# Performance work log

Hardware: AMD Instinct MI355X
Metric: run time of the kernel (lower is better)

The kernel has to match this reference:

```python
import jax, jax.numpy as jnp
import numpy as np

B, S, H, NS, HEADS, L = 16, 1024, 1024, 32, 16, 5
DH = H // HEADS
LN_EPS = 1e-7


def setup_inputs() -> dict:
    key = jax.random.key(0)
    ks = jax.random.split(key, 12)
    std = 0.02
    inp = {
        "encoder_layer": jax.random.normal(ks[0], (B, S, H), jnp.float32),
        "lstm_W_ih": jax.random.normal(ks[1], (4 * H, H), jnp.float32) * std,
        "lstm_W_hh": jax.random.normal(ks[2], (4 * H, H), jnp.float32) * std,
        "lstm_b_ih": jnp.zeros((4 * H,), jnp.float32),
        "lstm_b_hh": jnp.zeros((4 * H,), jnp.float32),
        "ln_gamma": jnp.ones((H,), jnp.float32),
        "ln_beta": jnp.zeros((H,), jnp.float32),
        "Wq": jax.random.normal(ks[3], (H, H), jnp.float32) * std,
        "bq": jnp.zeros((H,), jnp.float32),
        "Wk": jax.random.normal(ks[4], (H, H), jnp.float32) * std,
        "bk": jnp.zeros((H,), jnp.float32),
        "Wv": jax.random.normal(ks[5], (H, H), jnp.float32) * std,
        "bv": jnp.zeros((H,), jnp.float32),
        "Wo": jax.random.normal(ks[6], (H, H), jnp.float32) * std,
        "bo": jnp.zeros((H,), jnp.float32),
        "attn_ln_gamma": jnp.ones((H,), jnp.float32),
        "attn_ln_beta": jnp.zeros((H,), jnp.float32),
        "clf_W": jax.random.normal(ks[7], (L, H), jnp.float32) * std,
        "clf_b": jnp.zeros((L,), jnp.float32),
    }
    # contiguous ragged spans: head_j = 32*j, tail_j = 32*(j+1); slice is head+1:tail
    seg = S // NS
    heads = jnp.tile(jnp.arange(NS, dtype=jnp.int32)[None, :] * seg, (B, 1))
    inp["span_head_idxs"] = heads
    inp["span_tail_idxs"] = heads + seg
    inp["span_attention_mask"] = jnp.ones((B, NS), jnp.int32)
    return inp


def _layer_norm(x, gamma, beta):
    mu = jnp.mean(x, axis=-1, keepdims=True)
    var = jnp.mean(jnp.square(x - mu), axis=-1, keepdims=True)
    return (x - mu) * jax.lax.rsqrt(var + LN_EPS) * gamma + beta


def reference(encoder_layer, lstm_W_ih, lstm_W_hh, lstm_b_ih, lstm_b_hh,
              ln_gamma, ln_beta, Wq, bq, Wk, bk, Wv, bv, Wo, bo,
              attn_ln_gamma, attn_ln_beta, clf_W, clf_b,
              span_head_idxs, span_tail_idxs, span_attention_mask):
    # --- unidirectional LSTM over the sequence (torch gate order i,f,g,o) ---
    x_tbh = jnp.swapaxes(encoder_layer, 0, 1)  # [S,B,H]
    h0 = jnp.zeros((B, H), encoder_layer.dtype)
    c0 = jnp.zeros((B, H), encoder_layer.dtype)

    def step(carry, xt):
        h, c = carry
        gates = xt @ lstm_W_ih.T + lstm_b_ih + h @ lstm_W_hh.T + lstm_b_hh
        i, f, g, o = jnp.split(gates, 4, axis=-1)
        i, f, o = jax.nn.sigmoid(i), jax.nn.sigmoid(f), jax.nn.sigmoid(o)
        c = f * c + i * jnp.tanh(g)
        h = o * jnp.tanh(c)
        return (h, c), h

    _, hs = jax.lax.scan(step, (h0, c0), x_tbh)
    enc = jnp.swapaxes(hs, 0, 1)  # [B,S,H]

    # --- ragged span mean pooling (tokens head+1 .. tail-1) via masked matmul ---
    t = jnp.arange(S, dtype=jnp.int32)  # [S]
    span_mask = ((t[None, None, :] >= span_head_idxs[:, :, None] + 1)
                 & (t[None, None, :] < span_tail_idxs[:, :, None]))  # [B,NS,S]
    mf = span_mask.astype(enc.dtype)
    sums = jnp.einsum('bns,bsh->bnh', mf, enc)
    counts = jnp.sum(mf, axis=-1, keepdims=True)
    mean_vec = sums / counts  # [B,NS,H]

    mean_vec = _layer_norm(mean_vec, ln_gamma, ln_beta)

    # --- DeBERTa-style self-attention (relative_attention=False) over spans ---
    m2d = (span_attention_mask[:, None, None, :]
           * span_attention_mask[:, None, :, None])  # [B,1,NS,NS]
    mbool = m2d.astype(bool)

    def split_heads(y):
        return jnp.swapaxes(y.reshape(B, NS, HEADS, DH), 1, 2)  # [B,h,NS,dh]

    q = split_heads(mean_vec @ Wq.T + bq)
    k = split_heads(mean_vec @ Wk.T + bk)
    v = split_heads(mean_vec @ Wv.T + bv)
    scale = jnp.sqrt(jnp.asarray(DH, mean_vec.dtype))
    scores = jnp.einsum('bhqd,bhkd->bhqk', q, k) / scale
    scores = jnp.where(mbool, scores, jnp.finfo(scores.dtype).min)
    probs = jax.nn.softmax(scores, axis=-1)
    probs = jnp.where(mbool, probs, 0.0)  # XSoftmax zeroes masked positions
    ctx = jnp.einsum('bhqk,bhkd->bhqd', probs, v)
    ctx = jnp.swapaxes(ctx, 1, 2).reshape(B, NS, H)
    attn_out = _layer_norm(ctx @ Wo.T + bo + mean_vec, attn_ln_gamma, attn_ln_beta)

    # dropout is identity in eval mode
    logits = attn_out @ clf_W.T + clf_b  # [B,NS,L]
    return logits
```

## Files before the change

### kernel.cpp

```cpp
#include <hip/hip_runtime.h>
#include <hip/hip_bf16.h>

#define DEV __device__ __forceinline__

typedef __attribute__((ext_vector_type(8))) short short8;
typedef __attribute__((ext_vector_type(4))) float f32x4;
typedef __attribute__((ext_vector_type(4))) unsigned int u32x4;

static constexpr int B_ = 16, S_ = 1024, H_ = 1024, NS_ = 32, HEADS_ = 16, L_ = 5;
static constexpr int G4H = 4096;
static constexpr int LSTM_GRID = 64;

DEV unsigned short f2bf(float f){
  union { float f; unsigned int i; } u; u.f = f;
  unsigned int r = (u.i + 0x7fffu + ((u.i >> 16) & 1u)) >> 16;
  return (unsigned short)r;
}
DEV float bf2f(unsigned short h){
  union { unsigned int i; float f; } u; u.i = ((unsigned int)h) << 16;
  return u.f;
}
DEV float sigm(float x){ return 1.f / (1.f + __expf(-x)); }
DEV float tanh_(float x){
  x = fminf(30.f, fmaxf(-30.f, x));
  float e = __expf(-2.f * x);
  return (1.f - e) / (1.f + e);
}

DEV u32x4 load_coh16(const void* p){
  u32x4 r;
  asm volatile("global_load_dwordx4 %0, %1, off sc0 sc1" : "=v"(r) : "v"(p));
  return r;
}
DEV void store_coh16(void* p, u32x4 v){
  asm volatile("global_store_dwordx4 %0, %1, off sc0 sc1" :: "v"(p), "v"(v) : "memory");
}

__global__ void k_spanof(const int* __restrict__ head, const int* __restrict__ tail,
                         int* __restrict__ spanof){
  const int b = blockIdx.x;
  for (int t = threadIdx.x; t < S_; t += blockDim.x) spanof[b * S_ + t] = -1;
  __syncthreads();
  if (threadIdx.x < NS_){
    const int n = threadIdx.x;
    const int h = head[b * NS_ + n], tl = tail[b * NS_ + n];
    for (int t = h + 1; t < tl; ++t) spanof[b * S_ + t] = n;
  }
}

__global__ __launch_bounds__(256) void k_gates(const float* __restrict__ enc,
    const float* __restrict__ Wih, const float* __restrict__ bih,
    const float* __restrict__ bhh, unsigned short* __restrict__ gx){
  const int nb = blockIdx.x;
  const int mb = blockIdx.y;
  __shared__ __align__(16) unsigned short As[128 * 40];
  __shared__ __align__(16) unsigned short Bs[128 * 40];
  const int tid = threadIdx.x, w = tid >> 6, l = tid & 63;
  const int wm = (w >> 1) * 64, wn = (w & 1) * 64;
  const int cl = l & 15, bg = l >> 4;
  f32x4 acc[4][4] = {};
  const int t0 = mb * 8, n0 = nb * 128;
  const int srow = tid >> 1, skq = (tid & 1) * 16;
  const int sb = srow & 15, stt = t0 + (srow >> 4);
  const float* Asrc = enc + ((size_t)sb * S_ + stt) * H_ + skq;
  const float* Bsrc = Wih + (size_t)(n0 + srow) * H_ + skq;
  for (int k0 = 0; k0 < H_; k0 += 32){
    #pragma unroll
    for (int q = 0; q < 4; ++q){
      float4 a = *(const float4*)(Asrc + k0 + q * 4);
      float4 b = *(const float4*)(Bsrc + k0 + q * 4);
      ushort4 ua; ua.x = f2bf(a.x); ua.y = f2bf(a.y); ua.z = f2bf(a.z); ua.w = f2bf(a.w);
      ushort4 ub; ub.x = f2bf(b.x); ub.y = f2bf(b.y); ub.z = f2bf(b.z); ub.w = f2bf(b.w);
      *(ushort4*)(As + srow * 40 + skq + q * 4) = ua;
      *(ushort4*)(Bs + srow * 40 + skq + q * 4) = ub;
    }
    __syncthreads();
    short8 af[4], bf[4];
    const int kq = bg * 8;
    #pragma unroll
    for (int i = 0; i < 4; ++i) af[i] = *(const short8*)(As + (wm + i * 16 + cl) * 40 + kq);
    #pragma unroll
    for (int i = 0; i < 4; ++i) bf[i] = *(const short8*)(Bs + (wn + i * 16 + cl) * 40 + kq);
    #pragma unroll
    for (int mi = 0; mi < 4; ++mi)
      #pragma unroll
      for (int ni = 0; ni < 4; ++ni)
        acc[mi][ni] = __builtin_amdgcn_mfma_f32_16x16x32_bf16(af[mi], bf[ni], acc[mi][ni], 0, 0, 0);
    __syncthreads();
  }
  #pragma unroll
  for (int ni = 0; ni < 4; ++ni){
    const int c = n0 + wn + ni * 16 + cl;
    const float bias = bih[c] + bhh[c];
    const int g = c >> 10, j = c & 1023;
    const int cuq = j >> 4, wq = (j >> 2) & 3, jjq = j & 3;
    const int nq = jjq * 4 + g;
    #pragma unroll
    for (int mi = 0; mi < 4; ++mi){
      const int tg = t0 + ((wm + mi * 16) >> 4);
      ushort4 o;
      o.x = f2bf(acc[mi][ni].x + bias);
      o.y = f2bf(acc[mi][ni].y + bias);
      o.z = f2bf(acc[mi][ni].z + bias);
      o.w = f2bf(acc[mi][ni].w + bias);
      const size_t u4i = (((size_t)tg * 64 + cuq) * 64 + (wq * 16 + nq)) * 4 + bg;
      *((ushort4*)gx + u4i) = o;
    }
  }
}

__global__ __launch_bounds__(256, 1) void k_lstm(const float* __restrict__ Whh,
    const unsigned short* __restrict__ gx, const int* __restrict__ spanof,
    unsigned short* __restrict__ hbuf, unsigned int* __restrict__ tags,
    float* __restrict__ sums){
  __shared__ __align__(16) unsigned char Himg[32768];
  __shared__ __align__(16) unsigned short Hs[256];
  const int cu = blockIdx.x, tid = threadIdx.x;
  const int w = tid >> 6, l = tid & 63;
  const int n = l & 15, bg = l >> 4;
  const int g = n & 3, jj = n >> 2;
  const int j = cu * 16 + w * 4 + jj;
  const int bstar = bg * 4 + g;
  const int jl = w * 4 + jj;

  short8 wr[32];
  {
    const float* wsrc = Whh + (size_t)(g * H_ + j) * H_ + bg * 8;
    #pragma unroll
    for (int kk = 0; kk < 32; ++kk){
      float4 x = *(const float4*)(wsrc + kk * 32);
      float4 y = *(const float4*)(wsrc + kk * 32 + 4);
      short8 v;
      v[0] = (short)f2bf(x.x); v[1] = (short)f2bf(x.y);
      v[2] = (short)f2bf(x.z); v[3] = (short)f2bf(x.w);
      v[4] = (short)f2bf(y.x); v[5] = (short)f2bf(y.y);
      v[6] = (short)f2bf(y.z); v[7] = (short)f2bf(y.w);
      wr[kk] = v;
    }
  }

  const unsigned int abase = (unsigned)(n * 2048 + bg * 16);
  const unsigned int aswz  = (unsigned)((n & 7) << 4);

  const ushort4* gxp = (const ushort4*)gx + ((size_t)cu * 64 + w * 16 + n) * 4 + bg;
  const int* sp = spanof + (size_t)bstar * S_;

  float cstate = 0.f, pool = 0.f;
  int curspan = -1;

  for (int t = 0; t < S_; ++t){
    const int p = t & 1;
    const ushort4 gxv = gxp[(size_t)t * 16384];
    const int s = sp[t];
    {
      const unsigned int* tp = tags + (size_t)p * 1024 + (size_t)l * 16;
      unsigned int v = __hip_atomic_load(tp, __ATOMIC_RELAXED, __HIP_MEMORY_SCOPE_AGENT);
      int guard = 0;
      while (!__all(v == (unsigned int)t)){
        __builtin_amdgcn_s_sleep(1);
        v = __hip_atomic_load(tp, __ATOMIC_RELAXED, __HIP_MEMORY_SCOPE_AGENT);
        if (++guard > 2000000) break;
      }
    }
    {
      const unsigned char* hsrc = (const unsigned char*)hbuf + p * 32768 + w * 8192 + l * 16;
      u32x4 v0 = load_coh16(hsrc + 0 * 1024);
      u32x4 v1 = load_coh16(hsrc + 1 * 1024);
      u32x4 v2 = load_coh16(hsrc + 2 * 1024);
      u32x4 v3 = load_coh16(hsrc + 3 * 1024);
      u32x4 v4 = load_coh16(hsrc + 4 * 1024);
      u32x4 v5 = load_coh16(hsrc + 5 * 1024);
      u32x4 v6 = load_coh16(hsrc + 6 * 1024);
      u32x4 v7 = load_coh16(hsrc + 7 * 1024);
      asm volatile("s_waitcnt vmcnt(0)" ::: "memory");
      __builtin_amdgcn_sched_barrier(0);
      unsigned char* hdst = Himg + w * 8192 + l * 16;
      *(u32x4*)(hdst + 0 * 1024) = v0;
      *(u32x4*)(hdst + 1 * 1024) = v1;
      *(u32x4*)(hdst + 2 * 1024) = v2;
      *(u32x4*)(hdst + 3 * 1024) = v3;
      *(u32x4*)(hdst + 4 * 1024) = v4;
      *(u32x4*)(hdst + 5 * 1024) = v5;
      *(u32x4*)(hdst + 6 * 1024) = v6;
      *(u32x4*)(hdst + 7 * 1024) = v7;
    }
    __syncthreads();
    f32x4 a0 = {0,0,0,0}, a1 = {0,0,0,0}, a2 = {0,0,0,0}, a3 = {0,0,0,0};
    #pragma unroll
    for (int kk = 0; kk < 32; kk += 4){
      short8 h0 = *(const short8*)(Himg + ((abase + (kk + 0) * 64) ^ aswz));
      a0 = __builtin_amdgcn_mfma_f32_16x16x32_bf16(h0, wr[kk + 0], a0, 0, 0, 0);
      short8 h1 = *(const short8*)(Himg + ((abase + (kk + 1) * 64) ^ aswz));
      a1 = __builtin_amdgcn_mfma_f32_16x16x32_bf16(h1, wr[kk + 1], a1, 0, 0, 0);
      short8 h2 = *(const short8*)(Himg + ((abase + (kk + 2) * 64) ^ aswz));
      a2 = __builtin_amdgcn_mfma_f32_16x16x32_bf16(h2, wr[kk + 2], a2, 0, 0, 0);
      short8 h3 = *(const short8*)(Himg + ((abase + (kk + 3) * 64) ^ aswz));
      a3 = __builtin_amdgcn_mfma_f32_16x16x32_bf16(h3, wr[kk + 3], a3, 0, 0, 0);
    }
    f32x4 acc = (a0 + a1) + (a2 + a3);
    const float x0 = acc.x + bf2f(gxv.x);
    const float x1 = acc.y + bf2f(gxv.y);
    const float x2 = acc.z + bf2f(gxv.z);
    const float x3 = acc.w + bf2f(gxv.w);
    const float s1 = (g==0)?x1:(g==1)?x0:(g==2)?x3:x2;
    const float s2 = (g==0)?x2:(g==1)?x3:(g==2)?x0:x1;
    const float s3 = (g==0)?x3:(g==1)?x2:(g==2)?x1:x0;
    const float r1 = __shfl_xor(s1, 1, 64);
    const float r2 = __shfl_xor(s2, 2, 64);
    const float r3 = __shfl_xor(s3, 3, 64);
    const float own = (g==0)?x0:(g==1)?x1:(g==2)?x2:x3;
    const float vi = (g==0)?own:(g==1)?r1:(g==2)?r2:r3;
    const float vf = (g==1)?own:(g==0)?r1:(g==3)?r2:r3;
    const float vg = (g==2)?own:(g==3)?r1:(g==0)?r2:r3;
    const float vo = (g==3)?own:(g==2)?r1:(g==1)?r2:r3;
    const float ig = sigm(vi), fg = sigm(vf), gt = tanh_(vg), og = sigm(vo);
    cstate = fg * cstate + ig * gt;
    const float hval = og * tanh_(cstate);
    Hs[bstar * 16 + jl] = f2bf(hval);
    __syncthreads();
    if (tid < 32){
      const int sb = tid >> 1, half = tid & 1;
      const unsigned key = (unsigned)((sb & 7) << 4);
      const unsigned off = (unsigned)(sb * 2048)
          + ((unsigned)(cu * 32) ^ (key & 0x60))
          + ((unsigned)(half * 16) ^ (key & 0x10));
      u32x4 v = *(const u32x4*)((const unsigned char*)Hs + tid * 16);
      store_coh16((unsigned char*)hbuf + (p ^ 1) * 32768 + off, v);
    }
    if (tid == 0){
      asm volatile("s_waitcnt vmcnt(0)" ::: "memory");
      __hip_atomic_store(tags + (size_t)((t + 1) & 1) * 1024 + (size_t)cu * 16,
                         (unsigned int)(t + 1), __ATOMIC_RELAXED, __HIP_MEMORY_SCOPE_AGENT);
    }
    if (s != curspan){
      if (curspan >= 0) sums[((size_t)bstar * NS_ + curspan) * H_ + j] = pool;
      pool = 0.f; curspan = s;
    }
    if (s >= 0) pool += hval;
  }
  if (curspan >= 0) sums[((size_t)bstar * NS_ + curspan) * H_ + j] = pool;
}

DEV float block_sum(float v, float* red, int tid){
  #pragma unroll
  for (int d = 1; d < 64; d <<= 1) v += __shfl_xor(v, d, 64);
  if ((tid & 63) == 0) red[tid >> 6] = v;
  __syncthreads();
  const float r = red[0] + red[1] + red[2] + red[3];
  __syncthreads();
  return r;
}

__global__ __launch_bounds__(256) void k_poolln(const float* __restrict__ sums,
    const int* __restrict__ head, const int* __restrict__ tail,
    const float* __restrict__ gamma, const float* __restrict__ beta,
    unsigned short* __restrict__ mvb, float* __restrict__ mvf){
  __shared__ float red[4];
  const int m = blockIdx.x, tid = threadIdx.x;
  const float inv = 1.f / (float)(tail[m] - head[m] - 1);
  float4 x = *(const float4*)(sums + (size_t)m * H_ + tid * 4);
  x.x *= inv; x.y *= inv; x.z *= inv; x.w *= inv;
  const float mu = block_sum(x.x + x.y + x.z + x.w, red, tid) * (1.f / (float)H_);
  const float d0 = x.x - mu, d1 = x.y - mu, d2 = x.z - mu, d3 = x.w - mu;
  const float var = block_sum(d0*d0 + d1*d1 + d2*d2 + d3*d3, red, tid) * (1.f / (float)H_);
  const float rs = rsqrtf(var + 1e-7f);
  float4 gm = *(const float4*)(gamma + tid * 4);
  float4 bt = *(const float4*)(beta + tid * 4);
  float4 o; o.x = d0*rs*gm.x + bt.x; o.y = d1*rs*gm.y + bt.y;
  o.z = d2*rs*gm.z + bt.z; o.w = d3*rs*gm.w + bt.w;
  *(float4*)(mvf + (size_t)m * H_ + tid * 4) = o;
  ushort4 u; u.x = f2bf(o.x); u.y = f2bf(o.y); u.z = f2bf(o.z); u.w = f2bf(o.w);
  *(ushort4*)(mvb + (size_t)m * H_ + tid * 4) = u;
}

template<int OUT_BF16>
__global__ __launch_bounds__(256) void k_gemm2(const unsigned short* __restrict__ A,
    const float* __restrict__ Bw, const float* __restrict__ bias,
    float* __restrict__ Cf, unsigned short* __restrict__ Cb, int Nn){
  const int nb = blockIdx.x, mb = blockIdx.y;
  __shared__ __align__(16) unsigned short As[128 * 40];
  __shared__ __align__(16) unsigned short Bs[128 * 40];
  const int tid = threadIdx.x, w = tid >> 6, l = tid & 63;
  const int wm = (w >> 1) * 64, wn = (w & 1) * 64;
  const int cl = l & 15, bg = l >> 4;
  f32x4 acc[4][4] = {};
  const int m0 = mb * 128, n0 = nb * 128;
  const int srow = tid >> 1, skq = (tid & 1) * 16;
  const unsigned short* Asrc = A + (size_t)(m0 + srow) * 1024 + skq;
  const float* Bsrc = Bw + (size_t)(n0 + srow) * 1024 + skq;
  for (int k0 = 0; k0 < 1024; k0 += 32){
    uint4 av0 = *(const uint4*)(Asrc + k0);
    uint4 av1 = *(const uint4*)(Asrc + k0 + 8);
    *(uint4*)(As + srow * 40 + skq) = av0;
    *(uint4*)(As + srow * 40 + skq + 8) = av1;
    #pragma unroll
    for (int q = 0; q < 4; ++q){
      float4 b = *(const float4*)(Bsrc + k0 + q * 4);
      ushort4 ub; ub.x = f2bf(b.x); ub.y = f2bf(b.y); ub.z = f2bf(b.z); ub.w = f2bf(b.w);
      *(ushort4*)(Bs + srow * 40 + skq + q * 4) = ub;
    }
    __syncthreads();
    short8 af[4], bf[4];
    const int kq = bg * 8;
    #pragma unroll
    for (int i = 0; i < 4; ++i) af[i] = *(const short8*)(As + (wm + i * 16 + cl) * 40 + kq);
    #pragma unroll
    for (int i = 0; i < 4; ++i) bf[i] = *(const short8*)(Bs + (wn + i * 16 + cl) * 40 + kq);
    #pragma unroll
    for (int mi = 0; mi < 4; ++mi)
      #pragma unroll
      for (int ni = 0; ni < 4; ++ni)
        acc[mi][ni] = __builtin_amdgcn_mfma_f32_16x16x32_bf16(af[mi], bf[ni], acc[mi][ni], 0, 0, 0);
    __syncthreads();
  }
  #pragma unroll
  for (int ni = 0; ni < 4; ++ni){
    const int c = n0 + wn + ni * 16 + cl;
    const float bsv = bias ? bias[c] : 0.f;
    #pragma unroll
    for (int mi = 0; mi < 4; ++mi){
      const int m = m0 + wm + mi * 16 + bg * 4;
      const float v0 = acc[mi][ni].x + bsv, v1 = acc[mi][ni].y + bsv;
      const float v2 = acc[mi][ni].z + bsv, v3 = acc[mi][ni].w + bsv;
      if (OUT_BF16){
        Cb[(size_t)(m + 0) * Nn + c] = f2bf(v0);
        Cb[(size_t)(m + 1) * Nn + c] = f2bf(v1);
        Cb[(size_t)(m + 2) * Nn + c] = f2bf(v2);
        Cb[(size_t)(m + 3) * Nn + c] = f2bf(v3);
      } else {
        Cf[(size_t)(m + 0) * Nn + c] = v0;
        Cf[(size_t)(m + 1) * Nn + c] = v1;
        Cf[(size_t)(m + 2) * Nn + c] = v2;
        Cf[(size_t)(m + 3) * Nn + c] = v3;
      }
    }
  }
}

__global__ __launch_bounds__(256) void k_attn(const unsigned short* __restrict__ qb,
    const unsigned short* __restrict__ kb, const unsigned short* __restrict__ vb,
    const int* __restrict__ mask, unsigned short* __restrict__ ctx){
  const int bh = blockIdx.x, b = bh >> 4, hd = bh & 15;
  __shared__ float Q[32][64], K[32][64], V[32][64], Sc[32][33];
  __shared__ int msk[32];
  const int tid = threadIdx.x;
  const int row = tid >> 3, d0 = (tid & 7) * 8;
  {
    const size_t base = (size_t)(b * NS_ + row) * H_ + hd * 64 + d0;
    uint4 vq = *(const uint4*)(qb + base);
    uint4 vk = *(const uint4*)(kb + base);
    uint4 vv = *(const uint4*)(vb + base);
    const unsigned int wq[4] = {vq.x, vq.y, vq.z, vq.w};
    const unsigned int wk[4] = {vk.x, vk.y, vk.z, vk.w};
    const unsigned int wv[4] = {vv.x, vv.y, vv.z, vv.w};
    #pragma unroll
    for (int i = 0; i < 4; ++i){
      Q[row][d0 + 2*i]     = bf2f((unsigned short)(wq[i] & 0xffff));
      Q[row][d0 + 2*i + 1] = bf2f((unsigned short)(wq[i] >> 16));
      K[row][d0 + 2*i]     = bf2f((unsigned short)(wk[i] & 0xffff));
      K[row][d0 + 2*i + 1] = bf2f((unsigned short)(wk[i] >> 16));
      V[row][d0 + 2*i]     = bf2f((unsigned short)(wv[i] & 0xffff));
      V[row][d0 + 2*i + 1] = bf2f((unsigned short)(wv[i] >> 16));
    }
  }
  if (tid < 32) msk[tid] = mask[b * NS_ + tid];
  __syncthreads();
  {
    const int qi = tid >> 3, kb0 = (tid & 7) * 4;
    for (int kk = kb0; kk < kb0 + 4; ++kk){
      float s = 0.f;
      #pragma unroll
      for (int d = 0; d < 64; ++d) s += Q[qi][d] * K[kk][d];
      s *= 0.125f;
      if (!msk[qi] || !msk[kk]) s = -3.402823466e38f;
      Sc[qi][kk] = s;
    }
  }
  __syncthreads();
  if (tid < 32){
    float mx = -3.402823466e38f;
    for (int kk = 0; kk < 32; ++kk) mx = fmaxf(mx, Sc[tid][kk]);
    float sum = 0.f;
    for (int kk = 0; kk < 32; ++kk){
      const float e = __expf(Sc[tid][kk] - mx);
      Sc[tid][kk] = e; sum += e;
    }
    const float isum = 1.f / sum;
    for (int kk = 0; kk < 32; ++kk){
      float pv = Sc[tid][kk] * isum;
      if (!msk[tid] || !msk[kk]) pv = 0.f;
      Sc[tid][kk] = pv;
    }
  }
  __syncthreads();
  float o[8] = {0,0,0,0,0,0,0,0};
  for (int kk = 0; kk < 32; ++kk){
    const float p = Sc[row][kk];
    #pragma unroll
    for (int i = 0; i < 8; ++i) o[i] += p * V[kk][d0 + i];
  }
  ushort4 oA, oB;
  oA.x = f2bf(o[0]); oA.y = f2bf(o[1]); oA.z = f2bf(o[2]); oA.w = f2bf(o[3]);
  oB.x = f2bf(o[4]); oB.y = f2bf(o[5]); oB.z = f2bf(o[6]); oB.w = f2bf(o[7]);
  unsigned short* cp = ctx + (size_t)(b * NS_ + row) * H_ + hd * 64 + d0;
  *(ushort4*)(cp) = oA;
  *(ushort4*)(cp + 4) = oB;
}

__global__ __launch_bounds__(256) void k_residln(const float* __restrict__ wo,
    const float* __restrict__ mvf, const float* __restrict__ gamma,
    const float* __restrict__ beta, float* __restrict__ aof){
  __shared__ float red[4];
  const int m = blockIdx.x, tid = threadIdx.x;
  float4 a = *(const float4*)(wo + (size_t)m * H_ + tid * 4);
  float4 r = *(const float4*)(mvf + (size_t)m * H_ + tid * 4);
  float4 x; x.x = a.x + r.x; x.y = a.y + r.y; x.z = a.z + r.z; x.w = a.w + r.w;
  const float mu = block_sum(x.x + x.y + x.z + x.w, red, tid) * (1.f / (float)H_);
  const float d0 = x.x - mu, d1 = x.y - mu, d2 = x.z - mu, d3 = x.w - mu;
  const float var = block_sum(d0*d0 + d1*d1 + d2*d2 + d3*d3, red, tid) * (1.f / (float)H_);
  const float rs = rsqrtf(var + 1e-7f);
  float4 gm = *(const float4*)(gamma + tid * 4);
  float4 bt = *(const float4*)(beta + tid * 4);
  float4 o; o.x = d0*rs*gm.x + bt.x; o.y = d1*rs*gm.y + bt.y;
  o.z = d2*rs*gm.z + bt.z; o.w = d3*rs*gm.w + bt.w;
  *(float4*)(aof + (size_t)m * H_ + tid * 4) = o;
}

__global__ __launch_bounds__(64) void k_clf(const float* __restrict__ ao,
    const float* __restrict__ Wc, const float* __restrict__ bc, float* __restrict__ out){
  const int m = blockIdx.x, l = threadIdx.x;
  const float* a = ao + (size_t)m * H_ + l * 16;
  float av[16];
  #pragma unroll
  for (int i = 0; i < 4; ++i){
    float4 v = *(const float4*)(a + i * 4);
    av[i*4+0] = v.x; av[i*4+1] = v.y; av[i*4+2] = v.z; av[i*4+3] = v.w;
  }
  float p[5];
  #pragma unroll
  for (int c = 0; c < 5; ++c){
    const float* wr = Wc + (size_t)c * H_ + l * 16;
    float s = 0.f;
    #pragma unroll
    for (int i = 0; i < 4; ++i){
      float4 v = *(const float4*)(wr + i * 4);
      s += av[i*4+0]*v.x + av[i*4+1]*v.y + av[i*4+2]*v.z + av[i*4+3]*v.w;
    }
    p[c] = s;
  }
  #pragma unroll
  for (int d = 1; d < 64; d <<= 1){
    #pragma unroll
    for (int c = 0; c < 5; ++c) p[c] += __shfl_xor(p[c], d, 64);
  }
  if (l == 0){
    #pragma unroll
    for (int c = 0; c < 5; ++c) out[m * L_ + c] = p[c] + bc[c];
  }
}

extern "C" void kernel_launch(void* const* d_in, const int* in_sizes, int n_in,
                              void* d_out, int out_size, void* d_ws, size_t ws_size,
                              hipStream_t stream){
  (void)in_sizes; (void)n_in; (void)out_size; (void)ws_size;
  const float* enc  = (const float*)d_in[0];
  const float* Wih  = (const float*)d_in[1];
  const float* Whh  = (const float*)d_in[2];
  const float* bih  = (const float*)d_in[3];
  const float* bhh  = (const float*)d_in[4];
  const float* lng  = (const float*)d_in[5];
  const float* lnb  = (const float*)d_in[6];
  const float* Wq   = (const float*)d_in[7];
  const float* bq   = (const float*)d_in[8];
  const float* Wk   = (const float*)d_in[9];
  const float* bk   = (const float*)d_in[10];
  const float* Wv   = (const float*)d_in[11];
  const float* bv   = (const float*)d_in[12];
  const float* Wo   = (const float*)d_in[13];
  const float* bo   = (const float*)d_in[14];
  const float* alng = (const float*)d_in[15];
  const float* alnb = (const float*)d_in[16];
  const float* clfW = (const float*)d_in[17];
  const float* clfb = (const float*)d_in[18];
  const int* shead  = (const int*)d_in[19];
  const int* stail  = (const int*)d_in[20];
  const int* smask  = (const int*)d_in[21];
  float* out = (float*)d_out;
  unsigned char* ws = (unsigned char*)d_ws;

  size_t cur = 0;
  auto alloc = [&](size_t sz){ size_t r = cur; cur = (cur + sz + 255) & ~(size_t)255; return r; };
  const size_t off_gx   = alloc((size_t)S_ * G4H * B_ * 2);
  const size_t off_hbuf = alloc(2 * (size_t)B_ * H_ * 2);
  const size_t off_tags = alloc(2 * 1024 * 4);
  const size_t off_span = alloc((size_t)B_ * S_ * 4);
  const size_t off_sums = alloc((size_t)B_ * NS_ * H_ * 4);
  const size_t off_mvb  = alloc((size_t)B_ * NS_ * H_ * 2);
  const size_t off_mvf  = alloc((size_t)B_ * NS_ * H_ * 4);
  const size_t off_q    = alloc((size_t)B_ * NS_ * H_ * 2);
  const size_t off_k    = alloc((size_t)B_ * NS_ * H_ * 2);
  const size_t off_v    = alloc((size_t)B_ * NS_ * H_ * 2);
  const size_t off_ctx  = alloc((size_t)B_ * NS_ * H_ * 2);
  const size_t off_wo   = alloc((size_t)B_ * NS_ * H_ * 4);
  const size_t off_ao   = alloc((size_t)B_ * NS_ * H_ * 4);

  unsigned short* gx   = (unsigned short*)(ws + off_gx);
  unsigned short* hbuf = (unsigned short*)(ws + off_hbuf);
  unsigned int*   tags = (unsigned int*)(ws + off_tags);
  int*            span = (int*)(ws + off_span);
  float*          sums = (float*)(ws + off_sums);
  unsigned short* mvb  = (unsigned short*)(ws + off_mvb);
  float*          mvf  = (float*)(ws + off_mvf);
  unsigned short* qb   = (unsigned short*)(ws + off_q);
  unsigned short* kbp  = (unsigned short*)(ws + off_k);
  unsigned short* vbp  = (unsigned short*)(ws + off_v);
  unsigned short* ctx  = (unsigned short*)(ws + off_ctx);
  float*          wob  = (float*)(ws + off_wo);
  float*          aof  = (float*)(ws + off_ao);

  (void)hipMemsetAsync(hbuf, 0, 2 * (size_t)B_ * H_ * 2, stream);
  (void)hipMemsetAsync(tags, 0, 2 * 1024 * 4, stream);
  (void)hipMemsetAsync(sums, 0, (size_t)B_ * NS_ * H_ * 4, stream);

  k_spanof<<<B_, 256, 0, stream>>>(shead, stail, span);
  k_gates<<<dim3(32, 128), 256, 0, stream>>>(enc, Wih, bih, bhh, gx);

  k_lstm<<<LSTM_GRID, 256, 0, stream>>>(Whh, gx, span, hbuf, tags, sums);

  k_poolln<<<B_ * NS_, 256, 0, stream>>>(sums, shead, stail, lng, lnb, mvb, mvf);
  k_gemm2<1><<<dim3(8, 4), 256, 0, stream>>>(mvb, Wq, bq, nullptr, qb, 1024);
  k_gemm2<1><<<dim3(8, 4), 256, 0, stream>>>(mvb, Wk, bk, nullptr, kbp, 1024);
  k_gemm2<1><<<dim3(8, 4), 256, 0, stream>>>(mvb, Wv, bv, nullptr, vbp, 1024);
  k_attn<<<B_ * HEADS_, 256, 0, stream>>>(qb, kbp, vbp, smask, ctx);
  k_gemm2<0><<<dim3(8, 4), 256, 0, stream>>>(ctx, Wo, bo, wob, nullptr, 1024);
  k_residln<<<B_ * NS_, 256, 0, stream>>>(wob, mvf, alng, alnb, aof);
  k_clf<<<B_ * NS_, 64, 0, stream>>>(aof, clfW, clfb, out);
}
```

Before: 3.955 ms.

## Replace flag-then-load LSTM step sync with speculative load plus checksum validation

Each LSTM block now publishes its hidden-state slice contiguously, together with a tag carrying the step number and two checksums (a plain sum and a rotated sum) of the data it wrote. Consumers load the data and the tag in one round trip and retry until the checksums match. This removes the serialized sequence of polling a flag and then loading h, and drops the producer's wait for store completion before setting the flag. The cost is extra ALU and shuffle work per step, and correctness depends on checksums catching torn reads, which is probabilistic rather than guaranteed.

```diff
diff --git a/kernel.cpp b/kernel.cpp
--- a/kernel.cpp
+++ b/kernel.cpp
@@ -26,6 +26,7 @@
   float e = __expf(-2.f * x);
   return (1.f - e) / (1.f + e);
 }
+DEV unsigned rotl_(unsigned x, unsigned r){ r &= 31u; return r ? ((x << r) | (x >> (32 - r))) : x; }
 
 DEV u32x4 load_coh16(const void* p){
   u32x4 r;
@@ -111,7 +112,7 @@
 
 __global__ __launch_bounds__(256, 1) void k_lstm(const float* __restrict__ Whh,
     const unsigned short* __restrict__ gx, const int* __restrict__ spanof,
-    unsigned short* __restrict__ hbuf, unsigned int* __restrict__ tags,
+    unsigned short* __restrict__ hbuf, u32x4* __restrict__ tags,
     float* __restrict__ sums){
   __shared__ __align__(16) unsigned char Himg[32768];
   __shared__ __align__(16) unsigned short Hs[256];
@@ -142,6 +143,9 @@
   const unsigned int abase = (unsigned)(n * 2048 + bg * 16);
   const unsigned int aswz  = (unsigned)((n & 7) << 4);
 
+  const int cu_src = w * 16 + (l >> 2);
+  const int asub   = l & 3;
+
   const ushort4* gxp = (const ushort4*)gx + ((size_t)cu * 64 + w * 16 + n) * 4 + bg;
   const int* sp = spanof + (size_t)bstar * S_;
 
@@ -152,37 +156,52 @@
     const int p = t & 1;
     const ushort4 gxv = gxp[(size_t)t * 16384];
     const int s = sp[t];
+
+    u32x4 d0, d1, d2, d3, d4, d5, d6, d7;
     {
-      const unsigned int* tp = tags + (size_t)p * 1024 + (size_t)l * 16;
-      unsigned int v = __hip_atomic_load(tp, __ATOMIC_RELAXED, __HIP_MEMORY_SCOPE_AGENT);
-      int guard = 0;
-      while (!__all(v == (unsigned int)t)){
-        __builtin_amdgcn_s_sleep(1);
-        v = __hip_atomic_load(tp, __ATOMIC_RELAXED, __HIP_MEMORY_SCOPE_AGENT);
-        if (++guard > 2000000) break;
+      const unsigned char* dbase = (const unsigned char*)hbuf
+          + (size_t)p * 32768 + (size_t)cu_src * 512 + (size_t)asub * 128;
+      const u32x4* tagp = tags + (size_t)p * 64 + cu_src;
+      int rounds = 0;
+      for (;;){
+        d0 = load_coh16(dbase +   0);
+        d1 = load_coh16(dbase +  16);
+        d2 = load_coh16(dbase +  32);
+        d3 = load_coh16(dbase +  48);
+        d4 = load_coh16(dbase +  64);
+        d5 = load_coh16(dbase +  80);
+        d6 = load_coh16(dbase +  96);
+        d7 = load_coh16(dbase + 112);
+        u32x4 tg = load_coh16(tagp);
+        asm volatile("s_waitcnt vmcnt(0)" ::: "memory");
+        __builtin_amdgcn_sched_barrier(0);
+        const unsigned m0 = (unsigned)(asub * 8);
+        unsigned s0 = 0, s1 = 0;
+        const u32x4 dd[8] = {d0, d1, d2, d3, d4, d5, d6, d7};
+        #pragma unroll
+        for (int q = 0; q < 8; ++q){
+          const unsigned m = m0 + q;
+          s0 += dd[q].x + dd[q].y + dd[q].z + dd[q].w;
+          s1 += rotl_(dd[q].x, m) + rotl_(dd[q].y, m + 8)
+              + rotl_(dd[q].z, m + 16) + rotl_(dd[q].w, m + 24);
+        }
+        s0 += __shfl_xor(s0, 1, 64); s0 += __shfl_xor(s0, 2, 64);
+        s1 += __shfl_xor(s1, 1, 64); s1 += __shfl_xor(s1, 2, 64);
+        const bool ok = (tg.x == (unsigned)t) && (tg.y == s0) && (tg.z == s1);
+        if (__all(ok)) break;
+        if (++rounds > 200000) break;
       }
     }
     {
-      const unsigned char* hsrc = (const unsigned char*)hbuf + p * 32768 + w * 8192 + l * 16;
-      u32x4 v0 = load_coh16(hsrc + 0 * 1024);
-      u32x4 v1 = load_coh16(hsrc + 1 * 1024);
-      u32x4 v2 = load_coh16(hsrc + 2 * 1024);
-      u32x4 v3 = load_coh16(hsrc + 3 * 1024);
-      u32x4 v4 = load_coh16(hsrc + 4 * 1024);
-      u32x4 v5 = load_coh16(hsrc + 5 * 1024);
-      u32x4 v6 = load_coh16(hsrc + 6 * 1024);
-      u32x4 v7 = load_coh16(hsrc + 7 * 1024);
-      asm volatile("s_waitcnt vmcnt(0)" ::: "memory");
-      __builtin_amdgcn_sched_barrier(0);
-      unsigned char* hdst = Himg + w * 8192 + l * 16;
-      *(u32x4*)(hdst + 0 * 1024) = v0;
-      *(u32x4*)(hdst + 1 * 1024) = v1;
-      *(u32x4*)(hdst + 2 * 1024) = v2;
-      *(u32x4*)(hdst + 3 * 1024) = v3;
-      *(u32x4*)(hdst + 4 * 1024) = v4;
-      *(u32x4*)(hdst + 5 * 1024) = v5;
-      *(u32x4*)(hdst + 6 * 1024) = v6;
-      *(u32x4*)(hdst + 7 * 1024) = v7;
+      #pragma unroll
+      for (int q = 0; q < 8; ++q){
+        const int m = asub * 8 + q;
+        const int b = m >> 1;
+        unsigned addr = (unsigned)(b * 2048 + (cu_src * 16 + (m & 1) * 8) * 2);
+        addr ^= (unsigned)((b & 7) << 4);
+        const u32x4 dv = (q==0)?d0:(q==1)?d1:(q==2)?d2:(q==3)?d3:(q==4)?d4:(q==5)?d5:(q==6)?d6:d7;
+        *(u32x4*)(Himg + addr) = dv;
+      }
     }
     __syncthreads();
     f32x4 a0 = {0,0,0,0}, a1 = {0,0,0,0}, a2 = {0,0,0,0}, a3 = {0,0,0,0};
@@ -202,12 +221,12 @@
     const float x1 = acc.y + bf2f(gxv.y);
     const float x2 = acc.z + bf2f(gxv.z);
     const float x3 = acc.w + bf2f(gxv.w);
-    const float s1 = (g==0)?x1:(g==1)?x0:(g==2)?x3:x2;
-    const float s2 = (g==0)?x2:(g==1)?x3:(g==2)?x0:x1;
-    const float s3 = (g==0)?x3:(g==1)?x2:(g==2)?x1:x0;
-    const float r1 = __shfl_xor(s1, 1, 64);
-    const float r2 = __shfl_xor(s2, 2, 64);
-    const float r3 = __shfl_xor(s3, 3, 64);
+    const float s1v = (g==0)?x1:(g==1)?x0:(g==2)?x3:x2;
+    const float s2v = (g==0)?x2:(g==1)?x3:(g==2)?x0:x1;
+    const float s3v = (g==0)?x3:(g==1)?x2:(g==2)?x1:x0;
+    const float r1 = __shfl_xor(s1v, 1, 64);
+    const float r2 = __shfl_xor(s2v, 2, 64);
+    const float r3 = __shfl_xor(s3v, 3, 64);
     const float own = (g==0)?x0:(g==1)?x1:(g==2)?x2:x3;
     const float vi = (g==0)?own:(g==1)?r1:(g==2)?r2:r3;
     const float vf = (g==1)?own:(g==0)?r1:(g==3)?r2:r3;
@@ -218,19 +237,24 @@
     const float hval = og * tanh_(cstate);
     Hs[bstar * 16 + jl] = f2bf(hval);
     __syncthreads();
-    if (tid < 32){
-      const int sb = tid >> 1, half = tid & 1;
-      const unsigned key = (unsigned)((sb & 7) << 4);
-      const unsigned off = (unsigned)(sb * 2048)
-          + ((unsigned)(cu * 32) ^ (key & 0x60))
-          + ((unsigned)(half * 16) ^ (key & 0x10));
-      u32x4 v = *(const u32x4*)((const unsigned char*)Hs + tid * 16);
-      store_coh16((unsigned char*)hbuf + (p ^ 1) * 32768 + off, v);
-    }
-    if (tid == 0){
-      asm volatile("s_waitcnt vmcnt(0)" ::: "memory");
-      __hip_atomic_store(tags + (size_t)((t + 1) & 1) * 1024 + (size_t)cu * 16,
-                         (unsigned int)(t + 1), __ATOMIC_RELAXED, __HIP_MEMORY_SCOPE_AGENT);
+    if (w == 0){
+      u32x4 v = {0, 0, 0, 0};
+      if (tid < 32) v = *(const u32x4*)((const unsigned char*)Hs + tid * 16);
+      if (tid < 32)
+        store_coh16((unsigned char*)hbuf + (size_t)(p ^ 1) * 32768
+                    + (size_t)cu * 512 + (size_t)tid * 16, v);
+      unsigned c0 = v.x + v.y + v.z + v.w;
+      const unsigned i = (unsigned)tid;
+      unsigned c1 = rotl_(v.x, i) + rotl_(v.y, i + 8) + rotl_(v.z, i + 16) + rotl_(v.w, i + 24);
+      #pragma unroll
+      for (int d = 1; d < 64; d <<= 1){
+        c0 += __shfl_xor(c0, d, 64);
+        c1 += __shfl_xor(c1, d, 64);
+      }
+      if (tid == 0){
+        u32x4 tg; tg.x = (unsigned)(t + 1); tg.y = c0; tg.z = c1; tg.w = 0u;
+        store_coh16(tags + (size_t)((t + 1) & 1) * 64 + cu, tg);
+      }
     }
     if (s != curspan){
       if (curspan >= 0) sums[((size_t)bstar * NS_ + curspan) * H_ + j] = pool;
@@ -492,7 +516,7 @@
   auto alloc = [&](size_t sz){ size_t r = cur; cur = (cur + sz + 255) & ~(size_t)255; return r; };
   const size_t off_gx   = alloc((size_t)S_ * G4H * B_ * 2);
   const size_t off_hbuf = alloc(2 * (size_t)B_ * H_ * 2);
-  const size_t off_tags = alloc(2 * 1024 * 4);
+  const size_t off_tags = alloc(2 * 64 * 16);
   const size_t off_span = alloc((size_t)B_ * S_ * 4);
   const size_t off_sums = alloc((size_t)B_ * NS_ * H_ * 4);
   const size_t off_mvb  = alloc((size_t)B_ * NS_ * H_ * 2);
@@ -506,7 +530,7 @@
 
   unsigned short* gx   = (unsigned short*)(ws + off_gx);
   unsigned short* hbuf = (unsigned short*)(ws + off_hbuf);
-  unsigned int*   tags = (unsigned int*)(ws + off_tags);
+  u32x4*          tags = (u32x4*)(ws + off_tags);
   int*            span = (int*)(ws + off_span);
   float*          sums = (float*)(ws + off_sums);
   unsigned short* mvb  = (unsigned short*)(ws + off_mvb);
@@ -519,7 +543,7 @@
   float*          aof  = (float*)(ws + off_ao);
 
   (void)hipMemsetAsync(hbuf, 0, 2 * (size_t)B_ * H_ * 2, stream);
-  (void)hipMemsetAsync(tags, 0, 2 * 1024 * 4, stream);
+  (void)hipMemsetAsync(tags, 0, 2 * 64 * 16, stream);
   (void)hipMemsetAsync(sums, 0, (size_t)B_ * NS_ * H_ * 4, stream);
 
   k_spanof<<<B_, 256, 0, stream>>>(shead, stail, span);
```

New measurement: 6.254 ms. 58.1% more time.
